# Kernel tuning notes

Measured on AMD Instinct MI355X. Metric: run time of the kernel, lower is better.

## Reference

```python
import jax, jax.numpy as jnp
import numpy as np

N_NODES = 100000
N_EDGES = 1600000
IN_F = 64
HIDDEN = [64, 64, 32]


def _glorot(key, shape):
    limit = float(np.sqrt(6.0 / (shape[0] + shape[1])))
    return jax.random.uniform(key, shape, jnp.float32, -limit, limit)


def setup_inputs() -> dict:
    key = jax.random.key(0)
    ks = jax.random.split(key, 5)
    x = jax.random.normal(ks[0], (N_NODES, IN_F), jnp.float32)
    edge_index = jax.random.randint(ks[1], (2, N_EDGES), 0, N_NODES, jnp.int64)
    dims = [IN_F] + HIDDEN
    params = {}
    for i in range(len(HIDDEN)):
        params[f"W{i+1}"] = _glorot(ks[2 + i], (dims[i], dims[i + 1]))
        params[f"b{i+1}"] = jnp.zeros((dims[i + 1],), jnp.float32)
    return {"x": x, "edge_index": edge_index, **params}


def _gcn_layer(x, src, dst, norm, W, b, n):
    # PyG GCNConv: linear transform, then normalized scatter-sum aggregation, then bias
    h = x @ W                                  # [N, out]
    msg = norm[:, None] * h[src]               # gather + edge scaling, [E+N, out]
    out = jax.ops.segment_sum(msg, dst, num_segments=n)
    return out + b


def reference(x, edge_index, W1, b1, W2, b2, W3, b3):
    n = x.shape[0]
    # add self-loops (GCNConv default add_self_loops=True)
    loops = jnp.arange(n, dtype=edge_index.dtype)
    src = jnp.concatenate([edge_index[0], loops])
    dst = jnp.concatenate([edge_index[1], loops])
    # symmetric normalization: deg over destination (col), norm = d^-1/2[src]*d^-1/2[dst]
    deg = jax.ops.segment_sum(jnp.ones_like(src, x.dtype), dst, num_segments=n)
    dinv = jnp.where(deg > 0, jax.lax.rsqrt(deg), 0.0)
    norm = dinv[src] * dinv[dst]
    h = jax.nn.relu(_gcn_layer(x, src, dst, norm, W1, b1, n))
    h = jax.nn.relu(_gcn_layer(h, src, dst, norm, W2, b2, n))
    return _gcn_layer(h, src, dst, norm, W3, b3, n)
```

## Files before the change

### kernel.cpp

```cpp
#include <hip/hip_runtime.h>
#include <hip/hip_bf16.h>


#define BLOCK 256
#define NBUCKET 512
#define CHUNK 4096
#define SLOT 4608
#define MAX_NPB 256

typedef float f32x4 __attribute__((ext_vector_type(4)));
typedef short bf16x8 __attribute__((ext_vector_type(8)));

__device__ __forceinline__ float4 fma4(float s, float4 a, float4 b) {
  return make_float4(fmaf(s, a.x, b.x), fmaf(s, a.y, b.y),
                     fmaf(s, a.z, b.z), fmaf(s, a.w, b.w));
}

__device__ __forceinline__ unsigned int bf16r(float f) {
  unsigned int u = __float_as_uint(f);
  u += 0x7fffu + ((u >> 16) & 1u);
  return u >> 16;
}

__device__ __forceinline__ void bsplit(float v, unsigned int& h,
                                       unsigned int& l) {
  h = bf16r(v);
  float r = v - __uint_as_float(h << 16);
  l = bf16r(r);
}

__device__ __forceinline__ void acc_bf8(float4& lo, float4& hi, uint4 u) {
  lo.x += __uint_as_float(u.x << 16);
  lo.y += __uint_as_float(u.x & 0xffff0000u);
  lo.z += __uint_as_float(u.y << 16);
  lo.w += __uint_as_float(u.y & 0xffff0000u);
  hi.x += __uint_as_float(u.z << 16);
  hi.y += __uint_as_float(u.z & 0xffff0000u);
  hi.z += __uint_as_float(u.w << 16);
  hi.w += __uint_as_float(u.w & 0xffff0000u);
}


__global__ __launch_bounds__(BLOCK) void binning_kernel(
    const int* __restrict__ src, const int* __restrict__ dst,
    int* __restrict__ bcursor, int* __restrict__ binned, int e, int npb) {
  __shared__ int h[NBUCKET];
  __shared__ int base[NBUCKET];
  for (int i = threadIdx.x; i < NBUCKET; i += BLOCK) h[i] = 0;
  __syncthreads();
  const int cbase = blockIdx.x * CHUNK;
#pragma unroll
  for (int k = 0; k < CHUNK; k += BLOCK * 4) {
    int i = cbase + k + threadIdx.x * 4;
    if (i + 3 < e) {
      int4 d4 = *(const int4*)(dst + i);
      atomicAdd(&h[d4.x / npb], 1);
      atomicAdd(&h[d4.y / npb], 1);
      atomicAdd(&h[d4.z / npb], 1);
      atomicAdd(&h[d4.w / npb], 1);
    } else {
      for (int t = 0; t < 4; ++t)
        if (i + t < e) atomicAdd(&h[dst[i + t] / npb], 1);
    }
  }
  __syncthreads();
  for (int i = threadIdx.x; i < NBUCKET; i += BLOCK) {
    int c = h[i];
    base[i] = c ? atomicAdd(&bcursor[i], c) : 0;
    h[i] = 0;
  }
  __syncthreads();
#pragma unroll
  for (int k = 0; k < CHUNK; k += BLOCK * 4) {
    int i = cbase + k + threadIdx.x * 4;
    if (i + 3 < e) {
      int4 d4 = *(const int4*)(dst + i);
      int4 s4 = *(const int4*)(src + i);
      int b0 = d4.x / npb, b1 = d4.y / npb, b2 = d4.z / npb, b3 = d4.w / npb;
      int o0 = atomicAdd(&h[b0], 1);
      int o1 = atomicAdd(&h[b1], 1);
      int o2 = atomicAdd(&h[b2], 1);
      int o3 = atomicAdd(&h[b3], 1);
      binned[b0 * SLOT + base[b0] + o0] = s4.x | ((d4.x - b0 * npb) << 17);
      binned[b1 * SLOT + base[b1] + o1] = s4.y | ((d4.y - b1 * npb) << 17);
      binned[b2 * SLOT + base[b2] + o2] = s4.z | ((d4.z - b2 * npb) << 17);
      binned[b3 * SLOT + base[b3] + o3] = s4.w | ((d4.w - b3 * npb) << 17);
    } else {
      for (int t = 0; t < 4; ++t) {
        if (i + t < e) {
          int d = dst[i + t];
          int bkt = d / npb;
          int lofs = atomicAdd(&h[bkt], 1);
          binned[bkt * SLOT + base[bkt] + lofs] =
              src[i + t] | ((d - bkt * npb) << 17);
        }
      }
    }
  }
}

__global__ __launch_bounds__(BLOCK) void bucket_build(
    const int* __restrict__ binned, const int* __restrict__ bcursor,
    int* __restrict__ offs, int* __restrict__ cnt, float* __restrict__ dinv,
    int* __restrict__ csr_src, int n, int npb) {
  __shared__ int nhist[MAX_NPB];
  __shared__ int noff[MAX_NPB];
  __shared__ int lcsr[SLOT];
  const int b = blockIdx.x;
  const int node_base = b * npb;
  const int nodes = min(npb, n - node_base);
  if (nodes <= 0) return;
  const int ebase = b * SLOT;
  const int ecnt = bcursor[b];
  for (int i = threadIdx.x; i < npb; i += BLOCK) nhist[i] = 0;
  __syncthreads();
  for (int i = threadIdx.x; i < ecnt; i += BLOCK)
    atomicAdd(&nhist[binned[ebase + i] >> 17], 1);
  __syncthreads();
  if (threadIdx.x < 64) {
    const int lane = threadIdx.x;
    const int bi = lane * 4;
    int v0 = (bi + 0 < nodes) ? nhist[bi + 0] : 0;
    int v1 = (bi + 1 < nodes) ? nhist[bi + 1] : 0;
    int v2 = (bi + 2 < nodes) ? nhist[bi + 2] : 0;
    int v3 = (bi + 3 < nodes) ? nhist[bi + 3] : 0;
    int tsum = v0 + v1 + v2 + v3;
    int s = tsum;
#pragma unroll
    for (int o = 1; o < 64; o <<= 1) {
      int u = __shfl_up(s, o, 64);
      if (lane >= o) s += u;
    }
    int texcl = s - tsum;
    if (bi + 0 < nodes) noff[bi + 0] = texcl;
    if (bi + 1 < nodes) noff[bi + 1] = texcl + v0;
    if (bi + 2 < nodes) noff[bi + 2] = texcl + v0 + v1;
    if (bi + 3 < nodes) noff[bi + 3] = texcl + v0 + v1 + v2;
  }
  __syncthreads();
  for (int i = threadIdx.x; i < nodes; i += BLOCK) {
    int c = nhist[i];
    offs[node_base + i] = ebase + noff[i];
    cnt[node_base + i] = c;
    dinv[node_base + i] = rsqrtf((float)(c + 1));
  }
  __syncthreads();
  for (int i = threadIdx.x; i < ecnt; i += BLOCK) {
    int v = binned[ebase + i];
    int pos = atomicAdd(&noff[v >> 17], 1);
    lcsr[pos] = v & 0x1ffff;
  }
  __syncthreads();
  for (int i = threadIdx.x; i < ecnt; i += BLOCK)
    csr_src[ebase + i] = lcsr[i];
}

__global__ __launch_bounds__(BLOCK) void wprep_kernel(
    const float* __restrict__ W1, const float* __restrict__ W2,
    const float* __restrict__ W3, unsigned short* __restrict__ Wt) {
  int t = blockIdx.x * BLOCK + threadIdx.x;
  float v;
  int hi_off, lo_off;
  if (t < 4096) {
    int nn = t >> 6, k = t & 63;
    v = W1[k * 64 + nn];
    hi_off = t;
    lo_off = 4096 + t;
  } else if (t < 8192) {
    int i = t - 4096;
    int nn = i >> 6, k = i & 63;
    v = W2[k * 64 + nn];
    hi_off = 8192 + i;
    lo_off = 12288 + i;
  } else {
    int i = t - 8192;
    if (i >= 2048) return;
    int nn = i >> 6, k = i & 63;
    v = W3[k * 32 + nn];
    hi_off = 16384 + i;
    lo_off = 18432 + i;
  }
  unsigned int h, l;
  bsplit(v, h, l);
  Wt[hi_off] = (unsigned short)h;
  Wt[lo_off] = (unsigned short)l;
}


__global__ __launch_bounds__(BLOCK) void gemm1_kernel(
    const float* __restrict__ x, const unsigned short* __restrict__ Wt,
    const float* __restrict__ dinv, unsigned short* __restrict__ hbf, int n) {
  __shared__ unsigned short Ahi[16][72];
  __shared__ unsigned short Alo[16][72];
  __shared__ float dvs[16];
  const int r16 = threadIdx.x >> 4;
  const int c4 = (threadIdx.x & 15) * 4;
  const int node = blockIdx.x * 16 + r16;
  const int wv = threadIdx.x >> 6;
  const int fr = threadIdx.x & 15;
  const int fq = (threadIdx.x >> 4) & 3;
  const unsigned short* wb = Wt + ((wv * 16 + fr) * 64) + fq * 8;
  bf16x8 bh0 = *(const bf16x8*)(wb);
  bf16x8 bh1 = *(const bf16x8*)(wb + 32);
  bf16x8 bl0 = *(const bf16x8*)(wb + 4096);
  bf16x8 bl1 = *(const bf16x8*)(wb + 4096 + 32);
  uint2 ph = make_uint2(0u, 0u), pl = make_uint2(0u, 0u);
  if (node < n) {
    f32x4 xv =
        __builtin_nontemporal_load((const f32x4*)(x + (size_t)node * 64 + c4));
    unsigned int h0, l0, h1, l1, h2, l2, h3, l3;
    bsplit(xv.x, h0, l0);
    bsplit(xv.y, h1, l1);
    bsplit(xv.z, h2, l2);
    bsplit(xv.w, h3, l3);
    ph = make_uint2(h0 | (h1 << 16), h2 | (h3 << 16));
    pl = make_uint2(l0 | (l1 << 16), l2 | (l3 << 16));
  }
  *(uint2*)(&Ahi[r16][c4]) = ph;
  *(uint2*)(&Alo[r16][c4]) = pl;
  if ((threadIdx.x & 15) == 0) dvs[r16] = (node < n) ? dinv[node] : 0.f;
  __syncthreads();
  bf16x8 ah0 = *(const bf16x8*)(&Ahi[fr][fq * 8]);
  bf16x8 ah1 = *(const bf16x8*)(&Ahi[fr][fq * 8 + 32]);
  bf16x8 aL0 = *(const bf16x8*)(&Alo[fr][fq * 8]);
  bf16x8 aL1 = *(const bf16x8*)(&Alo[fr][fq * 8 + 32]);
  f32x4 acc = {0.f, 0.f, 0.f, 0.f};
  acc = __builtin_amdgcn_mfma_f32_16x16x32_bf16(ah0, bh0, acc, 0, 0, 0);
  acc = __builtin_amdgcn_mfma_f32_16x16x32_bf16(aL0, bh0, acc, 0, 0, 0);
  acc = __builtin_amdgcn_mfma_f32_16x16x32_bf16(ah0, bl0, acc, 0, 0, 0);
  acc = __builtin_amdgcn_mfma_f32_16x16x32_bf16(ah1, bh1, acc, 0, 0, 0);
  acc = __builtin_amdgcn_mfma_f32_16x16x32_bf16(aL1, bh1, acc, 0, 0, 0);
  acc = __builtin_amdgcn_mfma_f32_16x16x32_bf16(ah1, bl1, acc, 0, 0, 0);
  const int col = wv * 16 + fr;
#pragma unroll
  for (int j = 0; j < 4; ++j) {
    int row = fq * 4 + j;
    int nd = blockIdx.x * 16 + row;
    if (nd < n)
      hbf[(size_t)nd * 64 + col] = (unsigned short)bf16r(dvs[row] * acc[j]);
  }
}

__global__ __launch_bounds__(BLOCK) void fused_agg_gemm64(
    const unsigned short* __restrict__ hin, const int* __restrict__ csr_src,
    const int* __restrict__ offs, const int* __restrict__ cnt,
    const float* __restrict__ dinv, const float* __restrict__ bias,
    const unsigned short* __restrict__ Wt, unsigned short* __restrict__ hout,
    int n) {
  __shared__ unsigned short Ahi[16][72];
  __shared__ unsigned short Alo[16][72];
  __shared__ float dvs[16];
  const int g = threadIdx.x >> 4;
  const int lane16 = threadIdx.x & 15;
  const int colgrp = lane16 & 7;
  const int half = lane16 >> 3;
  const int c8 = colgrp * 8;
  const int node = blockIdx.x * 16 + g;
  const bool valid = node < n;
  float dnode = 0.f;
  uint4 qh = make_uint4(0u, 0u, 0u, 0u), ql = make_uint4(0u, 0u, 0u, 0u);
  if (valid) {
    const int start = offs[node];
    const int cn = cnt[node];
    const unsigned short* hcol = hin + c8;
    float4 l0 = make_float4(0.f, 0.f, 0.f, 0.f), h0 = l0;
    float4 l1 = l0, h1 = l0, l2 = l0, h2 = l0, l3 = l0, h3 = l0;
    if (half == 0)
      acc_bf8(l0, h0, *(const uint4*)(hcol + (size_t)node * 64));
    int j = half * 4;
    for (; j + 4 <= cn; j += 8) {
      int s0 = csr_src[start + j + 0];
      int s1 = csr_src[start + j + 1];
      int s2 = csr_src[start + j + 2];
      int s3 = csr_src[start + j + 3];
      uint4 u0 = *(const uint4*)(hcol + (size_t)s0 * 64);
      uint4 u1 = *(const uint4*)(hcol + (size_t)s1 * 64);
      uint4 u2 = *(const uint4*)(hcol + (size_t)s2 * 64);
      uint4 u3 = *(const uint4*)(hcol + (size_t)s3 * 64);
      acc_bf8(l0, h0, u0);
      acc_bf8(l1, h1, u1);
      acc_bf8(l2, h2, u2);
      acc_bf8(l3, h3, u3);
    }
    if (j < cn) {
      int rem = cn - j;
      int s0 = csr_src[start + j];
      acc_bf8(l1, h1, *(const uint4*)(hcol + (size_t)s0 * 64));
      if (rem > 1) {
        int s1 = csr_src[start + j + 1];
        acc_bf8(l2, h2, *(const uint4*)(hcol + (size_t)s1 * 64));
      }
      if (rem > 2) {
        int s2 = csr_src[start + j + 2];
        acc_bf8(l3, h3, *(const uint4*)(hcol + (size_t)s2 * 64));
      }
    }
    float4 alo = make_float4((l0.x + l1.x) + (l2.x + l3.x),
                             (l0.y + l1.y) + (l2.y + l3.y),
                             (l0.z + l1.z) + (l2.z + l3.z),
                             (l0.w + l1.w) + (l2.w + l3.w));
    float4 ahi = make_float4((h0.x + h1.x) + (h2.x + h3.x),
                             (h0.y + h1.y) + (h2.y + h3.y),
                             (h0.z + h1.z) + (h2.z + h3.z),
                             (h0.w + h1.w) + (h2.w + h3.w));
    alo.x += __shfl_xor(alo.x, 8); alo.y += __shfl_xor(alo.y, 8);
    alo.z += __shfl_xor(alo.z, 8); alo.w += __shfl_xor(alo.w, 8);
    ahi.x += __shfl_xor(ahi.x, 8); ahi.y += __shfl_xor(ahi.y, 8);
    ahi.z += __shfl_xor(ahi.z, 8); ahi.w += __shfl_xor(ahi.w, 8);
    dnode = dinv[node];
    if (half == 0) {
      float4 b4l = *(const float4*)(bias + c8);
      float4 b4h = *(const float4*)(bias + c8 + 4);
      float v0 = fmaxf(fmaf(dnode, alo.x, b4l.x), 0.f);
      float v1 = fmaxf(fmaf(dnode, alo.y, b4l.y), 0.f);
      float v2 = fmaxf(fmaf(dnode, alo.z, b4l.z), 0.f);
      float v3 = fmaxf(fmaf(dnode, alo.w, b4l.w), 0.f);
      float v4 = fmaxf(fmaf(dnode, ahi.x, b4h.x), 0.f);
      float v5 = fmaxf(fmaf(dnode, ahi.y, b4h.y), 0.f);
      float v6 = fmaxf(fmaf(dnode, ahi.z, b4h.z), 0.f);
      float v7 = fmaxf(fmaf(dnode, ahi.w, b4h.w), 0.f);
      unsigned int h0u, l0u, h1u, l1u, h2u, l2u, h3u, l3u;
      unsigned int h4u, l4u, h5u, l5u, h6u, l6u, h7u, l7u;
      bsplit(v0, h0u, l0u); bsplit(v1, h1u, l1u);
      bsplit(v2, h2u, l2u); bsplit(v3, h3u, l3u);
      bsplit(v4, h4u, l4u); bsplit(v5, h5u, l5u);
      bsplit(v6, h6u, l6u); bsplit(v7, h7u, l7u);
      qh = make_uint4(h0u | (h1u << 16), h2u | (h3u << 16),
                      h4u | (h5u << 16), h6u | (h7u << 16));
      ql = make_uint4(l0u | (l1u << 16), l2u | (l3u << 16),
                      l4u | (l5u << 16), l6u | (l7u << 16));
    }
  }
  if (half == 0) {
    *(uint4*)(&Ahi[g][c8]) = qh;
    *(uint4*)(&Alo[g][c8]) = ql;
    if (lane16 == 0) dvs[g] = dnode;
  }
  const int wv = threadIdx.x >> 6;
  const int fr = threadIdx.x & 15;
  const int fq = (threadIdx.x >> 4) & 3;
  const unsigned short* wb = Wt + ((wv * 16 + fr) * 64) + fq * 8;
  bf16x8 bh0 = *(const bf16x8*)(wb);
  bf16x8 bh1 = *(const bf16x8*)(wb + 32);
  bf16x8 bl0 = *(const bf16x8*)(wb + 4096);
  bf16x8 bl1 = *(const bf16x8*)(wb + 4096 + 32);
  __syncthreads();
  bf16x8 ah0 = *(const bf16x8*)(&Ahi[fr][fq * 8]);
  bf16x8 ah1 = *(const bf16x8*)(&Ahi[fr][fq * 8 + 32]);
  bf16x8 aL0 = *(const bf16x8*)(&Alo[fr][fq * 8]);
  bf16x8 aL1 = *(const bf16x8*)(&Alo[fr][fq * 8 + 32]);
  f32x4 acc = {0.f, 0.f, 0.f, 0.f};
  acc = __builtin_amdgcn_mfma_f32_16x16x32_bf16(ah0, bh0, acc, 0, 0, 0);
  acc = __builtin_amdgcn_mfma_f32_16x16x32_bf16(aL0, bh0, acc, 0, 0, 0);
  acc = __builtin_amdgcn_mfma_f32_16x16x32_bf16(ah0, bl0, acc, 0, 0, 0);
  acc = __builtin_amdgcn_mfma_f32_16x16x32_bf16(ah1, bh1, acc, 0, 0, 0);
  acc = __builtin_amdgcn_mfma_f32_16x16x32_bf16(aL1, bh1, acc, 0, 0, 0);
  acc = __builtin_amdgcn_mfma_f32_16x16x32_bf16(ah1, bl1, acc, 0, 0, 0);
  const int col = wv * 16 + fr;
#pragma unroll
  for (int j = 0; j < 4; ++j) {
    int row = fq * 4 + j;
    int nd = blockIdx.x * 16 + row;
    if (nd < n)
      hout[(size_t)nd * 64 + col] = (unsigned short)bf16r(dvs[row] * acc[j]);
  }
}

__global__ __launch_bounds__(BLOCK) void fused_agg_gemm32(
    const unsigned short* __restrict__ hin, const int* __restrict__ csr_src,
    const int* __restrict__ offs, const int* __restrict__ cnt,
    const float* __restrict__ dinv, const float* __restrict__ bias,
    const unsigned short* __restrict__ Wt, unsigned short* __restrict__ hout,
    int n) {
  __shared__ unsigned short Ahi[32][72];
  __shared__ unsigned short Alo[32][72];
  __shared__ float dvs[32];
  const int g = threadIdx.x >> 3;
  const int lane8 = threadIdx.x & 7;
  const int c8 = lane8 * 8;
  const int node = blockIdx.x * 32 + g;
  const bool valid = node < n;
  float dnode = 0.f;
  uint4 qh = make_uint4(0u, 0u, 0u, 0u), ql = make_uint4(0u, 0u, 0u, 0u);
  if (valid) {
    const int start = offs[node];
    const int cn = cnt[node];
    const unsigned short* hcol = hin + c8;
    float4 l0 = make_float4(0.f, 0.f, 0.f, 0.f), h0 = l0;
    float4 l1 = l0, h1 = l0, l2 = l0, h2 = l0, l3 = l0, h3 = l0;
    acc_bf8(l0, h0, *(const uint4*)(hcol + (size_t)node * 64));
    int j = 0;
    for (; j + 4 <= cn; j += 4) {
      int s0 = csr_src[start + j + 0];
      int s1 = csr_src[start + j + 1];
      int s2 = csr_src[start + j + 2];
      int s3 = csr_src[start + j + 3];
      uint4 u0 = *(const uint4*)(hcol + (size_t)s0 * 64);
      uint4 u1 = *(const uint4*)(hcol + (size_t)s1 * 64);
      uint4 u2 = *(const uint4*)(hcol + (size_t)s2 * 64);
      uint4 u3 = *(const uint4*)(hcol + (size_t)s3 * 64);
      acc_bf8(l0, h0, u0);
      acc_bf8(l1, h1, u1);
      acc_bf8(l2, h2, u2);
      acc_bf8(l3, h3, u3);
    }
    if (j + 2 <= cn) {
      int s0 = csr_src[start + j + 0];
      int s1 = csr_src[start + j + 1];
      uint4 u0 = *(const uint4*)(hcol + (size_t)s0 * 64);
      uint4 u1 = *(const uint4*)(hcol + (size_t)s1 * 64);
      acc_bf8(l1, h1, u0);
      acc_bf8(l2, h2, u1);
      j += 2;
    }
    if (j < cn) {
      int s0 = csr_src[start + j];
      acc_bf8(l3, h3, *(const uint4*)(hcol + (size_t)s0 * 64));
    }
    float4 alo = make_float4((l0.x + l1.x) + (l2.x + l3.x),
                             (l0.y + l1.y) + (l2.y + l3.y),
                             (l0.z + l1.z) + (l2.z + l3.z),
                             (l0.w + l1.w) + (l2.w + l3.w));
    float4 ahi = make_float4((h0.x + h1.x) + (h2.x + h3.x),
                             (h0.y + h1.y) + (h2.y + h3.y),
                             (h0.z + h1.z) + (h2.z + h3.z),
                             (h0.w + h1.w) + (h2.w + h3.w));
    dnode = dinv[node];
    float4 b4l = *(const float4*)(bias + c8);
    float4 b4h = *(const float4*)(bias + c8 + 4);
    float v0 = fmaxf(fmaf(dnode, alo.x, b4l.x), 0.f);
    float v1 = fmaxf(fmaf(dnode, alo.y, b4l.y), 0.f);
    float v2 = fmaxf(fmaf(dnode, alo.z, b4l.z), 0.f);
    float v3 = fmaxf(fmaf(dnode, alo.w, b4l.w), 0.f);
    float v4 = fmaxf(fmaf(dnode, ahi.x, b4h.x), 0.f);
    float v5 = fmaxf(fmaf(dnode, ahi.y, b4h.y), 0.f);
    float v6 = fmaxf(fmaf(dnode, ahi.z, b4h.z), 0.f);
    float v7 = fmaxf(fmaf(dnode, ahi.w, b4h.w), 0.f);
    unsigned int h0u, l0u, h1u, l1u, h2u, l2u, h3u, l3u;
    unsigned int h4u, l4u, h5u, l5u, h6u, l6u, h7u, l7u;
    bsplit(v0, h0u, l0u); bsplit(v1, h1u, l1u);
    bsplit(v2, h2u, l2u); bsplit(v3, h3u, l3u);
    bsplit(v4, h4u, l4u); bsplit(v5, h5u, l5u);
    bsplit(v6, h6u, l6u); bsplit(v7, h7u, l7u);
    qh = make_uint4(h0u | (h1u << 16), h2u | (h3u << 16),
                    h4u | (h5u << 16), h6u | (h7u << 16));
    ql = make_uint4(l0u | (l1u << 16), l2u | (l3u << 16),
                    l4u | (l5u << 16), l6u | (l7u << 16));
  }
  *(uint4*)(&Ahi[g][c8]) = qh;
  *(uint4*)(&Alo[g][c8]) = ql;
  if (lane8 == 0) dvs[g] = dnode;
  const int wv = threadIdx.x >> 6;
  const int mt = wv >> 1;
  const int nt = wv & 1;
  const int fr = threadIdx.x & 15;
  const int fq = (threadIdx.x >> 4) & 3;
  const unsigned short* wb = Wt + ((nt * 16 + fr) * 64) + fq * 8;
  bf16x8 bh0 = *(const bf16x8*)(wb);
  bf16x8 bh1 = *(const bf16x8*)(wb + 32);
  bf16x8 bl0 = *(const bf16x8*)(wb + 2048);
  bf16x8 bl1 = *(const bf16x8*)(wb + 2048 + 32);
  __syncthreads();
  bf16x8 ah0 = *(const bf16x8*)(&Ahi[mt * 16 + fr][fq * 8]);
  bf16x8 ah1 = *(const bf16x8*)(&Ahi[mt * 16 + fr][fq * 8 + 32]);
  bf16x8 aL0 = *(const bf16x8*)(&Alo[mt * 16 + fr][fq * 8]);
  bf16x8 aL1 = *(const bf16x8*)(&Alo[mt * 16 + fr][fq * 8 + 32]);
  f32x4 acc = {0.f, 0.f, 0.f, 0.f};
  acc = __builtin_amdgcn_mfma_f32_16x16x32_bf16(ah0, bh0, acc, 0, 0, 0);
  acc = __builtin_amdgcn_mfma_f32_16x16x32_bf16(aL0, bh0, acc, 0, 0, 0);
  acc = __builtin_amdgcn_mfma_f32_16x16x32_bf16(ah0, bl0, acc, 0, 0, 0);
  acc = __builtin_amdgcn_mfma_f32_16x16x32_bf16(ah1, bh1, acc, 0, 0, 0);
  acc = __builtin_amdgcn_mfma_f32_16x16x32_bf16(aL1, bh1, acc, 0, 0, 0);
  acc = __builtin_amdgcn_mfma_f32_16x16x32_bf16(ah1, bl1, acc, 0, 0, 0);
  const int col = nt * 16 + fr;
#pragma unroll
  for (int j = 0; j < 4; ++j) {
    int row = mt * 16 + fq * 4 + j;
    int nd = blockIdx.x * 32 + row;
    if (nd < n)
      hout[(size_t)nd * 32 + col] = (unsigned short)bf16r(dvs[row] * acc[j]);
  }
}

__global__ __launch_bounds__(BLOCK) void agg3_kernel(
    const unsigned short* __restrict__ hbf, const int* __restrict__ csr_src,
    const int* __restrict__ offs, const int* __restrict__ cnt,
    const float* __restrict__ dinv, const float* __restrict__ bias,
    float* __restrict__ out, int n) {
  constexpr int F = 32;
  const int node = blockIdx.x * 64 + (int)(threadIdx.x >> 2);
  const int c8 = (threadIdx.x & 3) * 8;
  if (node >= n) return;
  const int start = offs[node];
  const int cn = cnt[node];
  const unsigned short* hcol = hbf + c8;
  float4 l0 = make_float4(0.f, 0.f, 0.f, 0.f), h0 = l0;
  float4 l1 = l0, h1 = l0, l2 = l0, h2 = l0, l3 = l0, h3 = l0;
  acc_bf8(l0, h0, *(const uint4*)(hcol + (size_t)node * F));
  int j = 0;
  for (; j + 4 <= cn; j += 4) {
    int s0 = csr_src[start + j + 0];
    int s1 = csr_src[start + j + 1];
    int s2 = csr_src[start + j + 2];
    int s3 = csr_src[start + j + 3];
    uint4 u0 = *(const uint4*)(hcol + (size_t)s0 * F);
    uint4 u1 = *(const uint4*)(hcol + (size_t)s1 * F);
    uint4 u2 = *(const uint4*)(hcol + (size_t)s2 * F);
    uint4 u3 = *(const uint4*)(hcol + (size_t)s3 * F);
    acc_bf8(l0, h0, u0);
    acc_bf8(l1, h1, u1);
    acc_bf8(l2, h2, u2);
    acc_bf8(l3, h3, u3);
  }
  if (j + 2 <= cn) {
    int s0 = csr_src[start + j + 0];
    int s1 = csr_src[start + j + 1];
    uint4 u0 = *(const uint4*)(hcol + (size_t)s0 * F);
    uint4 u1 = *(const uint4*)(hcol + (size_t)s1 * F);
    acc_bf8(l1, h1, u0);
    acc_bf8(l2, h2, u1);
    j += 2;
  }
  if (j < cn) {
    int s0 = csr_src[start + j];
    acc_bf8(l3, h3, *(const uint4*)(hcol + (size_t)s0 * F));
  }
  float4 alo = make_float4((l0.x + l1.x) + (l2.x + l3.x),
                           (l0.y + l1.y) + (l2.y + l3.y),
                           (l0.z + l1.z) + (l2.z + l3.z),
                           (l0.w + l1.w) + (l2.w + l3.w));
  float4 ahi = make_float4((h0.x + h1.x) + (h2.x + h3.x),
                           (h0.y + h1.y) + (h2.y + h3.y),
                           (h0.z + h1.z) + (h2.z + h3.z),
                           (h0.w + h1.w) + (h2.w + h3.w));
  float d = dinv[node];
  float4 blo = *(const float4*)(bias + c8);
  float4 bhi = *(const float4*)(bias + c8 + 4);
  f32x4 vlo = {fmaf(d, alo.x, blo.x), fmaf(d, alo.y, blo.y),
               fmaf(d, alo.z, blo.z), fmaf(d, alo.w, blo.w)};
  f32x4 vhi = {fmaf(d, ahi.x, bhi.x), fmaf(d, ahi.y, bhi.y),
               fmaf(d, ahi.z, bhi.z), fmaf(d, ahi.w, bhi.w)};
  float* op = out + (size_t)node * F + c8;
  __builtin_nontemporal_store(vlo, (f32x4*)op);
  __builtin_nontemporal_store(vhi, (f32x4*)(op + 4));
}

static inline size_t align_up(size_t v, size_t a) { return (v + a - 1) & ~(a - 1); }

extern "C" void kernel_launch(void* const* d_in, const int* in_sizes, int n_in,
                              void* d_out, int out_size, void* d_ws, size_t ws_size,
                              hipStream_t stream) {
  const float* x = (const float*)d_in[0];
  const int* edge_index = (const int*)d_in[1];
  const float* W1 = (const float*)d_in[2];
  const float* b1 = (const float*)d_in[3];
  const float* W2 = (const float*)d_in[4];
  const float* b2 = (const float*)d_in[5];
  const float* W3 = (const float*)d_in[6];
  const float* b3 = (const float*)d_in[7];
  float* out = (float*)d_out;

  const int n = in_sizes[0] / 64;
  const int e = in_sizes[1] / 2;
  const int* e_src = edge_index;
  const int* e_dst = edge_index + e;
  const int npb = (n + NBUCKET - 1) / NBUCKET;

  char* ws = (char*)d_ws;
  size_t off = 0;
  int* bcursor = (int*)(ws + off); off = align_up(off + NBUCKET * 4, 512);
  int* offs    = (int*)(ws + off); off = align_up(off + (size_t)n * 4, 512);
  int* cnt     = (int*)(ws + off); off = align_up(off + (size_t)n * 4, 512);
  float* dinv  = (float*)(ws + off); off = align_up(off + (size_t)n * 4, 512);
  int* binned  = (int*)(ws + off); off = align_up(off + (size_t)NBUCKET * SLOT * 4, 512);
  int* csr_src = (int*)(ws + off); off = align_up(off + (size_t)NBUCKET * SLOT * 4, 512);
  unsigned short* hbuf_a = (unsigned short*)(ws + off);
  off = align_up(off + (size_t)n * 64 * 2, 512);
  unsigned short* hbuf_b = (unsigned short*)(ws + off);
  off = align_up(off + (size_t)n * 64 * 2, 512);
  unsigned short* Wt = (unsigned short*)(ws + off);
  off = align_up(off + (size_t)20480 * 2, 512);
  (void)ws_size;

  unsigned short* Wt1 = Wt;
  unsigned short* Wt2 = Wt + 8192;
  unsigned short* Wt3 = Wt + 16384;

  const int gC = (e + CHUNK - 1) / CHUNK;

  hipMemsetAsync(bcursor, 0, NBUCKET * 4, stream);
  wprep_kernel<<<40, BLOCK, 0, stream>>>(W1, W2, W3, Wt);
  binning_kernel<<<gC, BLOCK, 0, stream>>>(e_src, e_dst, bcursor, binned, e, npb);
  bucket_build<<<NBUCKET, BLOCK, 0, stream>>>(binned, bcursor, offs, cnt, dinv,
                                              csr_src, n, npb);

  gemm1_kernel<<<(n + 15) / 16, BLOCK, 0, stream>>>(x, Wt1, dinv, hbuf_a, n);
  fused_agg_gemm64<<<(n + 15) / 16, BLOCK, 0, stream>>>(
      hbuf_a, csr_src, offs, cnt, dinv, b1, Wt2, hbuf_b, n);
  fused_agg_gemm32<<<(n + 31) / 32, BLOCK, 0, stream>>>(
      hbuf_b, csr_src, offs, cnt, dinv, b2, Wt3, hbuf_a, n);
  agg3_kernel<<<(n + 63) / 64, BLOCK, 0, stream>>>(hbuf_a, csr_src, offs, cnt,
                                                   dinv, b3, out, n);
}
```

Before: 242.8 us.

## Pad per-node CSR segments to multiples of four with zero-row sentinel

Each node's CSR edge list is padded up to a multiple of four entries, with the padding filled by a sentinel index n that points at a zero row appended to each feature buffer. The aggregation loops then load four source indices with one int4 read and drop their remainder tail branches. Addresses are now formed with 32-bit shifts instead of size_t multiplies. The cost is extra zero-row gathers per node, one more feature row in each buffer, and a silent clamp if the padded total exceeds SLOT.

Result: faster. 236.1 us (-2.7%).

```diff
diff --git a/kernel.cpp b/kernel.cpp
--- a/kernel.cpp
+++ b/kernel.cpp
@@ -10,11 +10,6 @@
 
 typedef float f32x4 __attribute__((ext_vector_type(4)));
 typedef short bf16x8 __attribute__((ext_vector_type(8)));
-
-__device__ __forceinline__ float4 fma4(float s, float4 a, float4 b) {
-  return make_float4(fmaf(s, a.x, b.x), fmaf(s, a.y, b.y),
-                     fmaf(s, a.z, b.z), fmaf(s, a.w, b.w));
-}
 
 __device__ __forceinline__ unsigned int bf16r(float f) {
   unsigned int u = __float_as_uint(f);
@@ -106,6 +101,7 @@
   __shared__ int nhist[MAX_NPB];
   __shared__ int noff[MAX_NPB];
   __shared__ int lcsr[SLOT];
+  __shared__ int ptot_sh;
   const int b = blockIdx.x;
   const int node_base = b * npb;
   const int nodes = min(npb, n - node_base);
@@ -124,7 +120,11 @@
     int v1 = (bi + 1 < nodes) ? nhist[bi + 1] : 0;
     int v2 = (bi + 2 < nodes) ? nhist[bi + 2] : 0;
     int v3 = (bi + 3 < nodes) ? nhist[bi + 3] : 0;
-    int tsum = v0 + v1 + v2 + v3;
+    int p0 = (v0 + 3) & ~3;
+    int p1 = (v1 + 3) & ~3;
+    int p2 = (v2 + 3) & ~3;
+    int p3 = (v3 + 3) & ~3;
+    int tsum = p0 + p1 + p2 + p3;
     int s = tsum;
 #pragma unroll
     for (int o = 1; o < 64; o <<= 1) {
@@ -133,17 +133,20 @@
     }
     int texcl = s - tsum;
     if (bi + 0 < nodes) noff[bi + 0] = texcl;
-    if (bi + 1 < nodes) noff[bi + 1] = texcl + v0;
-    if (bi + 2 < nodes) noff[bi + 2] = texcl + v0 + v1;
-    if (bi + 3 < nodes) noff[bi + 3] = texcl + v0 + v1 + v2;
-  }
-  __syncthreads();
+    if (bi + 1 < nodes) noff[bi + 1] = texcl + p0;
+    if (bi + 2 < nodes) noff[bi + 2] = texcl + p0 + p1;
+    if (bi + 3 < nodes) noff[bi + 3] = texcl + p0 + p1 + p2;
+    if (lane == 63) ptot_sh = s;
+  }
+  __syncthreads();
+  const int ptot = min(ptot_sh, SLOT);
   for (int i = threadIdx.x; i < nodes; i += BLOCK) {
     int c = nhist[i];
     offs[node_base + i] = ebase + noff[i];
     cnt[node_base + i] = c;
     dinv[node_base + i] = rsqrtf((float)(c + 1));
   }
+  for (int i = threadIdx.x; i < ptot; i += BLOCK) lcsr[i] = n;
   __syncthreads();
   for (int i = threadIdx.x; i < ecnt; i += BLOCK) {
     int v = binned[ebase + i];
@@ -151,7 +154,7 @@
     lcsr[pos] = v & 0x1ffff;
   }
   __syncthreads();
-  for (int i = threadIdx.x; i < ecnt; i += BLOCK)
+  for (int i = threadIdx.x; i < ptot; i += BLOCK)
     csr_src[ebase + i] = lcsr[i];
 }
 
@@ -193,6 +196,9 @@
   __shared__ unsigned short Ahi[16][72];
   __shared__ unsigned short Alo[16][72];
   __shared__ float dvs[16];
+  if (blockIdx.x == 0 && threadIdx.x < 8)
+    *(uint4*)(hbf + (size_t)n * 64 + threadIdx.x * 8) =
+        make_uint4(0u, 0u, 0u, 0u);
   const int r16 = threadIdx.x >> 4;
   const int c4 = (threadIdx.x & 15) * 4;
   const int node = blockIdx.x * 16 + r16;
@@ -250,6 +256,9 @@
   __shared__ unsigned short Ahi[16][72];
   __shared__ unsigned short Alo[16][72];
   __shared__ float dvs[16];
+  if (blockIdx.x == 0 && threadIdx.x < 8)
+    *(uint4*)(hout + (size_t)n * 64 + threadIdx.x * 8) =
+        make_uint4(0u, 0u, 0u, 0u);
   const int g = threadIdx.x >> 4;
   const int lane16 = threadIdx.x & 15;
   const int colgrp = lane16 & 7;
@@ -259,41 +268,25 @@
   const bool valid = node < n;
   float dnode = 0.f;
   uint4 qh = make_uint4(0u, 0u, 0u, 0u), ql = make_uint4(0u, 0u, 0u, 0u);
+  const char* hbase = (const char*)hin + c8 * 2;
   if (valid) {
     const int start = offs[node];
     const int cn = cnt[node];
-    const unsigned short* hcol = hin + c8;
+    const int* cp = csr_src + start;
     float4 l0 = make_float4(0.f, 0.f, 0.f, 0.f), h0 = l0;
     float4 l1 = l0, h1 = l0, l2 = l0, h2 = l0, l3 = l0, h3 = l0;
     if (half == 0)
-      acc_bf8(l0, h0, *(const uint4*)(hcol + (size_t)node * 64));
-    int j = half * 4;
-    for (; j + 4 <= cn; j += 8) {
-      int s0 = csr_src[start + j + 0];
-      int s1 = csr_src[start + j + 1];
-      int s2 = csr_src[start + j + 2];
-      int s3 = csr_src[start + j + 3];
-      uint4 u0 = *(const uint4*)(hcol + (size_t)s0 * 64);
-      uint4 u1 = *(const uint4*)(hcol + (size_t)s1 * 64);
-      uint4 u2 = *(const uint4*)(hcol + (size_t)s2 * 64);
-      uint4 u3 = *(const uint4*)(hcol + (size_t)s3 * 64);
+      acc_bf8(l0, h0, *(const uint4*)(hbase + ((unsigned)node << 7)));
+    for (int j = half * 4; j < cn; j += 8) {
+      int4 sv = *(const int4*)(cp + j);
+      uint4 u0 = *(const uint4*)(hbase + ((unsigned)sv.x << 7));
+      uint4 u1 = *(const uint4*)(hbase + ((unsigned)sv.y << 7));
+      uint4 u2 = *(const uint4*)(hbase + ((unsigned)sv.z << 7));
+      uint4 u3 = *(const uint4*)(hbase + ((unsigned)sv.w << 7));
       acc_bf8(l0, h0, u0);
       acc_bf8(l1, h1, u1);
       acc_bf8(l2, h2, u2);
       acc_bf8(l3, h3, u3);
-    }
-    if (j < cn) {
-      int rem = cn - j;
-      int s0 = csr_src[start + j];
-      acc_bf8(l1, h1, *(const uint4*)(hcol + (size_t)s0 * 64));
-      if (rem > 1) {
-        int s1 = csr_src[start + j + 1];
-        acc_bf8(l2, h2, *(const uint4*)(hcol + (size_t)s1 * 64));
-      }
-      if (rem > 2) {
-        int s2 = csr_src[start + j + 2];
-        acc_bf8(l3, h3, *(const uint4*)(hcol + (size_t)s2 * 64));
-      }
     }
     float4 alo = make_float4((l0.x + l1.x) + (l2.x + l3.x),
                              (l0.y + l1.y) + (l2.y + l3.y),
@@ -375,6 +368,9 @@
   __shared__ unsigned short Ahi[32][72];
   __shared__ unsigned short Alo[32][72];
   __shared__ float dvs[32];
+  if (blockIdx.x == 0 && threadIdx.x < 4)
+    *(uint4*)(hout + (size_t)n * 32 + threadIdx.x * 8) =
+        make_uint4(0u, 0u, 0u, 0u);
   const int g = threadIdx.x >> 3;
   const int lane8 = threadIdx.x & 7;
   const int c8 = lane8 * 8;
@@ -382,40 +378,24 @@
   const bool valid = node < n;
   float dnode = 0.f;
   uint4 qh = make_uint4(0u, 0u, 0u, 0u), ql = make_uint4(0u, 0u, 0u, 0u);
+  const char* hbase = (const char*)hin + c8 * 2;
   if (valid) {
     const int start = offs[node];
     const int cn = cnt[node];
-    const unsigned short* hcol = hin + c8;
+    const int* cp = csr_src + start;
     float4 l0 = make_float4(0.f, 0.f, 0.f, 0.f), h0 = l0;
     float4 l1 = l0, h1 = l0, l2 = l0, h2 = l0, l3 = l0, h3 = l0;
-    acc_bf8(l0, h0, *(const uint4*)(hcol + (size_t)node * 64));
-    int j = 0;
-    for (; j + 4 <= cn; j += 4) {
-      int s0 = csr_src[start + j + 0];
-      int s1 = csr_src[start + j + 1];
-      int s2 = csr_src[start + j + 2];
-      int s3 = csr_src[start + j + 3];
-      uint4 u0 = *(const uint4*)(hcol + (size_t)s0 * 64);
-      uint4 u1 = *(const uint4*)(hcol + (size_t)s1 * 64);
-      uint4 u2 = *(const uint4*)(hcol + (size_t)s2 * 64);
-      uint4 u3 = *(const uint4*)(hcol + (size_t)s3 * 64);
+    acc_bf8(l0, h0, *(const uint4*)(hbase + ((unsigned)node << 7)));
+    for (int j = 0; j < cn; j += 4) {
+      int4 sv = *(const int4*)(cp + j);
+      uint4 u0 = *(const uint4*)(hbase + ((unsigned)sv.x << 7));
+      uint4 u1 = *(const uint4*)(hbase + ((unsigned)sv.y << 7));
+      uint4 u2 = *(const uint4*)(hbase + ((unsigned)sv.z << 7));
+      uint4 u3 = *(const uint4*)(hbase + ((unsigned)sv.w << 7));
       acc_bf8(l0, h0, u0);
       acc_bf8(l1, h1, u1);
       acc_bf8(l2, h2, u2);
       acc_bf8(l3, h3, u3);
-    }
-    if (j + 2 <= cn) {
-      int s0 = csr_src[start + j + 0];
-      int s1 = csr_src[start + j + 1];
-      uint4 u0 = *(const uint4*)(hcol + (size_t)s0 * 64);
-      uint4 u1 = *(const uint4*)(hcol + (size_t)s1 * 64);
-      acc_bf8(l1, h1, u0);
-      acc_bf8(l2, h2, u1);
-      j += 2;
-    }
-    if (j < cn) {
-      int s0 = csr_src[start + j];
-      acc_bf8(l3, h3, *(const uint4*)(hcol + (size_t)s0 * 64));
     }
     float4 alo = make_float4((l0.x + l1.x) + (l2.x + l3.x),
                              (l0.y + l1.y) + (l2.y + l3.y),
@@ -493,37 +473,21 @@
   if (node >= n) return;
   const int start = offs[node];
   const int cn = cnt[node];
-  const unsigned short* hcol = hbf + c8;
+  const int* cp = csr_src + start;
+  const char* hbase = (const char*)hbf + c8 * 2;
   float4 l0 = make_float4(0.f, 0.f, 0.f, 0.f), h0 = l0;
   float4 l1 = l0, h1 = l0, l2 = l0, h2 = l0, l3 = l0, h3 = l0;
-  acc_bf8(l0, h0, *(const uint4*)(hcol + (size_t)node * F));
-  int j = 0;
-  for (; j + 4 <= cn; j += 4) {
-    int s0 = csr_src[start + j + 0];
-    int s1 = csr_src[start + j + 1];
-    int s2 = csr_src[start + j + 2];
-    int s3 = csr_src[start + j + 3];
-    uint4 u0 = *(const uint4*)(hcol + (size_t)s0 * F);
-    uint4 u1 = *(const uint4*)(hcol + (size_t)s1 * F);
-    uint4 u2 = *(const uint4*)(hcol + (size_t)s2 * F);
-    uint4 u3 = *(const uint4*)(hcol + (size_t)s3 * F);
+  acc_bf8(l0, h0, *(const uint4*)(hbase + ((unsigned)node << 6)));
+  for (int j = 0; j < cn; j += 4) {
+    int4 sv = *(const int4*)(cp + j);
+    uint4 u0 = *(const uint4*)(hbase + ((unsigned)sv.x << 6));
+    uint4 u1 = *(const uint4*)(hbase + ((unsigned)sv.y << 6));
+    uint4 u2 = *(const uint4*)(hbase + ((unsigned)sv.z << 6));
+    uint4 u3 = *(const uint4*)(hbase + ((unsigned)sv.w << 6));
     acc_bf8(l0, h0, u0);
     acc_bf8(l1, h1, u1);
     acc_bf8(l2, h2, u2);
     acc_bf8(l3, h3, u3);
-  }
-  if (j + 2 <= cn) {
-    int s0 = csr_src[start + j + 0];
-    int s1 = csr_src[start + j + 1];
-    uint4 u0 = *(const uint4*)(hcol + (size_t)s0 * F);
-    uint4 u1 = *(const uint4*)(hcol + (size_t)s1 * F);
-    acc_bf8(l1, h1, u0);
-    acc_bf8(l2, h2, u1);
-    j += 2;
-  }
-  if (j < cn) {
-    int s0 = csr_src[start + j];
-    acc_bf8(l3, h3, *(const uint4*)(hcol + (size_t)s0 * F));
   }
   float4 alo = make_float4((l0.x + l1.x) + (l2.x + l3.x),
                            (l0.y + l1.y) + (l2.y + l3.y),
@@ -575,9 +539,9 @@
   int* binned  = (int*)(ws + off); off = align_up(off + (size_t)NBUCKET * SLOT * 4, 512);
   int* csr_src = (int*)(ws + off); off = align_up(off + (size_t)NBUCKET * SLOT * 4, 512);
   unsigned short* hbuf_a = (unsigned short*)(ws + off);
-  off = align_up(off + (size_t)n * 64 * 2, 512);
+  off = align_up(off + (size_t)(n + 1) * 64 * 2, 512);
   unsigned short* hbuf_b = (unsigned short*)(ws + off);
-  off = align_up(off + (size_t)n * 64 * 2, 512);
+  off = align_up(off + (size_t)(n + 1) * 64 * 2, 512);
   unsigned short* Wt = (unsigned short*)(ws + off);
   off = align_up(off + (size_t)20480 * 2, 512);
   (void)ws_size;
```
